# Kernel optimization log

Hardware: AMD Instinct MI355X
Metric: run time of the kernel (lower is better)

## Reference

```python
import jax, jax.numpy as jnp
import numpy as np

FP8_MAX = 448.0  # max finite value of float8_e4m3fn


def setup_inputs() -> dict:
    key = jax.random.key(0)
    k1, k2, k3 = jax.random.split(key, 3)
    T, H = 8192, 4096
    x = jax.random.normal(k1, (T, H), dtype=jnp.float32)
    w = jax.random.uniform(k2, (H, H), dtype=jnp.float32)  # stored as fp8 in the module; quantized in reference
    wscale = jax.random.uniform(k3, (1,), dtype=jnp.float32)
    return {"x": x, "w": w, "wscale": wscale}


def reference(x, w, wscale):
    # Dynamic per-token activation quantization to fp8 e4m3 (symmetric).
    x_scale = jnp.max(jnp.abs(x), axis=-1, keepdims=True) / FP8_MAX  # [T, 1]
    x_scale = jnp.maximum(x_scale, jnp.float32(1e-12))
    x_q = jnp.clip(x / x_scale, -FP8_MAX, FP8_MAX).astype(jnp.float8_e4m3fn)
    # Weight is stored in fp8 (per-tensor scale wscale); replicate the cast.
    w_q = w.astype(jnp.float8_e4m3fn)
    # Scaled fp8 matmul with fp32 accumulation, then dequant by x_scale * wscale.
    y = jnp.einsum('tk,kh->th', x_q.astype(jnp.float32), w_q.astype(jnp.float32))
    y = y * x_scale * wscale  # [T, H]
    # tensor_model_parallel_all_reduce is identity on a single device.
    return y
```

## Files before the change

kernel.cpp:

```cpp
#include <hip/hip_runtime.h>
#include <stdint.h>

#define T_DIM 8192
#define K_DIM 4096
#define N_DIM 4096
#define FP8MAX 448.0f

typedef __attribute__((ext_vector_type(4))) float floatx4;
typedef __attribute__((ext_vector_type(2))) long longx2;


__device__ static inline void load16_g2lds(const void* gptr, void* lptr) {
    __builtin_amdgcn_global_load_lds(
        (const __attribute__((address_space(1))) void*)gptr,
        (__attribute__((address_space(3))) void*)lptr,
        16, 0, 0);
}

__device__ static inline uint32_t pack4_fp8(float f0, float f1, float f2, float f3) {
    int p = 0;
    p = __builtin_amdgcn_cvt_pk_fp8_f32(f0, f1, p, false);
    p = __builtin_amdgcn_cvt_pk_fp8_f32(f2, f3, p, true);
    return (uint32_t)p;
}

__global__ __launch_bounds__(256) void xquant_kernel(
    const float* __restrict__ x, uint8_t* __restrict__ xq,
    float* __restrict__ xscale)
{
    const int t = blockIdx.x;
    const int tid = threadIdx.x;
    const int lane = tid & 63;
    const int wave = tid >> 6;
    const float4* xr4 = (const float4*)(x + (size_t)t * K_DIM);

    float4 v[4];
    float m = 0.0f;
#pragma unroll
    for (int e = 0; e < 4; ++e) {
        v[e] = xr4[tid + e * 256];
        m = fmaxf(m, fmaxf(fmaxf(fabsf(v[e].x), fabsf(v[e].y)),
                           fmaxf(fabsf(v[e].z), fabsf(v[e].w))));
    }
#pragma unroll
    for (int off = 32; off > 0; off >>= 1)
        m = fmaxf(m, __shfl_down(m, off, 64));
    __shared__ float red[4];
    if (lane == 0) red[wave] = m;
    __syncthreads();
    float mm = fmaxf(fmaxf(red[0], red[1]), fmaxf(red[2], red[3]));
    float scale = fmaxf(mm / FP8MAX, 1e-12f);
    if (tid == 0) xscale[t] = scale;
    const float inv = 1.0f / scale;

    uint32_t* xqr = (uint32_t*)(xq + (size_t)t * K_DIM);
#pragma unroll
    for (int e = 0; e < 4; ++e) {
        float q0 = fminf(fmaxf(v[e].x * inv, -FP8MAX), FP8MAX);
        float q1 = fminf(fmaxf(v[e].y * inv, -FP8MAX), FP8MAX);
        float q2 = fminf(fmaxf(v[e].z * inv, -FP8MAX), FP8MAX);
        float q3 = fminf(fmaxf(v[e].w * inv, -FP8MAX), FP8MAX);
        xqr[tid + e * 256] = pack4_fp8(q0, q1, q2, q3);
    }
}

__global__ __launch_bounds__(256) void wquant_kernel(
    const float* __restrict__ w, uint8_t* __restrict__ wqT)
{
    const int n0 = blockIdx.x * 64;
    const int k0 = blockIdx.y * 64;
    __shared__ __align__(4) uint8_t tile[64][68];

#pragma unroll
    for (int e = 0; e < 4; ++e) {
        int idx = threadIdx.x + e * 256;
        int r = idx >> 4;
        int c4 = idx & 15;
        float4 v = *(const float4*)(w + (size_t)(k0 + r) * N_DIM + n0 + c4 * 4);
        uint32_t p = pack4_fp8(v.x, v.y, v.z, v.w);
        tile[c4 * 4 + 0][r] = (uint8_t)(p);
        tile[c4 * 4 + 1][r] = (uint8_t)(p >> 8);
        tile[c4 * 4 + 2][r] = (uint8_t)(p >> 16);
        tile[c4 * 4 + 3][r] = (uint8_t)(p >> 24);
    }
    __syncthreads();
#pragma unroll
    for (int e = 0; e < 4; ++e) {
        int idx = threadIdx.x + e * 256;
        int rr = idx >> 4;
        int cc = idx & 15;
        uint32_t u = *(const uint32_t*)&tile[rr][cc * 4];
        *(uint32_t*)(wqT + (size_t)(n0 + rr) * K_DIM + k0 + cc * 4) = u;
    }
}

__global__ __launch_bounds__(256) void gemm_fp8_kernel(
    const uint8_t* __restrict__ xq, const uint8_t* __restrict__ wqT,
    const float* __restrict__ xscale, const float* __restrict__ wscale,
    float* __restrict__ out)
{
    __shared__ __align__(16) uint8_t As[128 * 64];
    __shared__ __align__(16) uint8_t Bs[128 * 64];

    const int tid = threadIdx.x;
    const int lane = tid & 63;
    const int wave = tid >> 6;
    const int m0 = blockIdx.y * 128;
    const int n0 = blockIdx.x * 128;
    const int wm = (wave >> 1) * 64;
    const int wn = (wave & 1) * 64;
    const int row = lane & 15;
    const int quad = lane >> 4;

    floatx4 acc[4][4] = {{{0.f,0.f,0.f,0.f}}};

    const int c0 = tid, c1 = tid + 256;
    const int r0 = c0 >> 2, g0 = (c0 & 3) ^ (r0 & 3);
    const int r1 = c1 >> 2, g1 = (c1 & 3) ^ (r1 & 3);
    const uint8_t* gA0 = xq  + (size_t)(m0 + r0) * K_DIM + g0 * 16;
    const uint8_t* gA1 = xq  + (size_t)(m0 + r1) * K_DIM + g1 * 16;
    const uint8_t* gB0 = wqT + (size_t)(n0 + r0) * K_DIM + g0 * 16;
    const uint8_t* gB1 = wqT + (size_t)(n0 + r1) * K_DIM + g1 * 16;
    uint8_t* lA0 = As + c0 * 16;
    uint8_t* lA1 = As + c1 * 16;
    uint8_t* lB0 = Bs + c0 * 16;
    uint8_t* lB1 = Bs + c1 * 16;

    int aoff[4], boff[4];
#pragma unroll
    for (int i = 0; i < 4; ++i) {
        const int mr = wm + i * 16 + row;
        const int nr = wn + i * 16 + row;
        aoff[i] = mr * 64 + ((quad ^ (mr & 3)) << 4);
        boff[i] = nr * 64 + ((quad ^ (nr & 3)) << 4);
    }

    for (int k0 = 0; k0 < K_DIM; k0 += 64) {
        __syncthreads();
        load16_g2lds(gA0 + k0, lA0);
        load16_g2lds(gA1 + k0, lA1);
        load16_g2lds(gB0 + k0, lB0);
        load16_g2lds(gB1 + k0, lB1);
        __syncthreads();

        longx2 a[4], b[4];
#pragma unroll
        for (int i = 0; i < 4; ++i) a[i] = *(const longx2*)(As + aoff[i]);
#pragma unroll
        for (int j = 0; j < 4; ++j) b[j] = *(const longx2*)(Bs + boff[j]);
#pragma unroll
        for (int i = 0; i < 4; ++i)
#pragma unroll
            for (int j = 0; j < 4; ++j) {
                acc[i][j] = __builtin_amdgcn_mfma_f32_16x16x32_fp8_fp8(
                    a[i].x, b[j].x, acc[i][j], 0, 0, 0);
                acc[i][j] = __builtin_amdgcn_mfma_f32_16x16x32_fp8_fp8(
                    a[i].y, b[j].y, acc[i][j], 0, 0, 0);
            }
    }

    const float wsv = wscale[0];
#pragma unroll
    for (int i = 0; i < 4; ++i) {
        const int rbase = m0 + wm + i * 16 + quad * 4;
        float s[4];
#pragma unroll
        for (int r = 0; r < 4; ++r) s[r] = xscale[rbase + r] * wsv;
#pragma unroll
        for (int j = 0; j < 4; ++j) {
            const int col = n0 + wn + j * 16 + row;
#pragma unroll
            for (int r = 0; r < 4; ++r)
                out[(size_t)(rbase + r) * N_DIM + col] = acc[i][j][r] * s[r];
        }
    }
}


extern "C" void kernel_launch(void* const* d_in, const int* in_sizes, int n_in,
                              void* d_out, int out_size, void* d_ws, size_t ws_size,
                              hipStream_t stream) {
    const float* x      = (const float*)d_in[0];
    const float* w      = (const float*)d_in[1];
    const float* wscale = (const float*)d_in[2];
    float* out = (float*)d_out;

    uint8_t* xq  = (uint8_t*)d_ws;
    uint8_t* wqT = xq + (size_t)T_DIM * K_DIM;
    float* xscale = (float*)(wqT + (size_t)N_DIM * K_DIM);

    xquant_kernel<<<T_DIM, 256, 0, stream>>>(x, xq, xscale);
    wquant_kernel<<<dim3(N_DIM / 64, K_DIM / 64), 256, 0, stream>>>(w, wqT);
    gemm_fp8_kernel<<<dim3(N_DIM / 128, T_DIM / 128), 256, 0, stream>>>(
        xq, wqT, xscale, wscale, out);
}
```

Baseline: 473.5 us.

## Use gfx950 16x16x128 scaled MFMA with 128-wide K tiles and faster weight transpose

Replaces the pair of 16x16x32 fp8 MFMAs with a single 16x16x128 scaled f8f6f4 MFMA (unit scales 0x7F), doubling the K tile to 128 and widening the LDS swizzle to 8 groups. It also rewrites the weight quantize/transpose to store packed words into LDS and transpose bytes in registers, avoiding byte-wise LDS stores. The aim is higher MFMA throughput and fewer barriers per K step, at the cost of doubled LDS use per block, which may lower occupancy.

```diff
diff --git a/kernel.cpp b/kernel.cpp
--- a/kernel.cpp
+++ b/kernel.cpp
@@ -7,7 +7,8 @@
 #define FP8MAX 448.0f
 
 typedef __attribute__((ext_vector_type(4))) float floatx4;
-typedef __attribute__((ext_vector_type(2))) long longx2;
+typedef __attribute__((ext_vector_type(4))) int   intx4;
+typedef __attribute__((ext_vector_type(8))) int   intx8;
 
 
 __device__ static inline void load16_g2lds(const void* gptr, void* lptr) {
@@ -69,7 +70,7 @@
 {
     const int n0 = blockIdx.x * 64;
     const int k0 = blockIdx.y * 64;
-    __shared__ __align__(4) uint8_t tile[64][68];
+    __shared__ uint32_t tile[64][17];
 
 #pragma unroll
     for (int e = 0; e < 4; ++e) {
@@ -77,20 +78,22 @@
         int r = idx >> 4;
         int c4 = idx & 15;
         float4 v = *(const float4*)(w + (size_t)(k0 + r) * N_DIM + n0 + c4 * 4);
-        uint32_t p = pack4_fp8(v.x, v.y, v.z, v.w);
-        tile[c4 * 4 + 0][r] = (uint8_t)(p);
-        tile[c4 * 4 + 1][r] = (uint8_t)(p >> 8);
-        tile[c4 * 4 + 2][r] = (uint8_t)(p >> 16);
-        tile[c4 * 4 + 3][r] = (uint8_t)(p >> 24);
+        tile[r][c4] = pack4_fp8(v.x, v.y, v.z, v.w);
     }
     __syncthreads();
-#pragma unroll
-    for (int e = 0; e < 4; ++e) {
-        int idx = threadIdx.x + e * 256;
-        int rr = idx >> 4;
-        int cc = idx & 15;
-        uint32_t u = *(const uint32_t*)&tile[rr][cc * 4];
-        *(uint32_t*)(wqT + (size_t)(n0 + rr) * K_DIM + k0 + cc * 4) = u;
+    const int kg = threadIdx.x & 15;
+    const int ng = threadIdx.x >> 4;
+    uint32_t in0 = tile[kg * 4 + 0][ng];
+    uint32_t in1 = tile[kg * 4 + 1][ng];
+    uint32_t in2 = tile[kg * 4 + 2][ng];
+    uint32_t in3 = tile[kg * 4 + 3][ng];
+#pragma unroll
+    for (int i = 0; i < 4; ++i) {
+        uint32_t o = ((in0 >> (8 * i)) & 0xFFu)
+                   | (((in1 >> (8 * i)) & 0xFFu) << 8)
+                   | (((in2 >> (8 * i)) & 0xFFu) << 16)
+                   | (((in3 >> (8 * i)) & 0xFFu) << 24);
+        *(uint32_t*)(wqT + (size_t)(n0 + ng * 4 + i) * K_DIM + k0 + kg * 4) = o;
     }
 }
 
@@ -99,8 +102,8 @@
     const float* __restrict__ xscale, const float* __restrict__ wscale,
     float* __restrict__ out)
 {
-    __shared__ __align__(16) uint8_t As[128 * 64];
-    __shared__ __align__(16) uint8_t Bs[128 * 64];
+    __shared__ __align__(16) uint8_t As[128 * 128];
+    __shared__ __align__(16) uint8_t Bs[128 * 128];
 
     const int tid = threadIdx.x;
     const int lane = tid & 63;
@@ -114,49 +117,62 @@
 
     floatx4 acc[4][4] = {{{0.f,0.f,0.f,0.f}}};
 
-    const int c0 = tid, c1 = tid + 256;
-    const int r0 = c0 >> 2, g0 = (c0 & 3) ^ (r0 & 3);
-    const int r1 = c1 >> 2, g1 = (c1 & 3) ^ (r1 & 3);
-    const uint8_t* gA0 = xq  + (size_t)(m0 + r0) * K_DIM + g0 * 16;
-    const uint8_t* gA1 = xq  + (size_t)(m0 + r1) * K_DIM + g1 * 16;
-    const uint8_t* gB0 = wqT + (size_t)(n0 + r0) * K_DIM + g0 * 16;
-    const uint8_t* gB1 = wqT + (size_t)(n0 + r1) * K_DIM + g1 * 16;
-    uint8_t* lA0 = As + c0 * 16;
-    uint8_t* lA1 = As + c1 * 16;
-    uint8_t* lB0 = Bs + c0 * 16;
-    uint8_t* lB1 = Bs + c1 * 16;
-
-    int aoff[4], boff[4];
+    const uint8_t* gA[4];
+    const uint8_t* gB[4];
+    uint8_t* lA[4];
+    uint8_t* lB[4];
+#pragma unroll
+    for (int p = 0; p < 4; ++p) {
+        const int c = tid + p * 256;
+        const int r = c >> 3, gg = c & 7, g = gg ^ (r & 7);
+        gA[p] = xq  + (size_t)(m0 + r) * K_DIM + g * 16;
+        gB[p] = wqT + (size_t)(n0 + r) * K_DIM + g * 16;
+        lA[p] = As + c * 16;
+        lB[p] = Bs + c * 16;
+    }
+
+    int aoff0[4], aoff1[4], boff0[4], boff1[4];
 #pragma unroll
     for (int i = 0; i < 4; ++i) {
         const int mr = wm + i * 16 + row;
         const int nr = wn + i * 16 + row;
-        aoff[i] = mr * 64 + ((quad ^ (mr & 3)) << 4);
-        boff[i] = nr * 64 + ((quad ^ (nr & 3)) << 4);
-    }
-
-    for (int k0 = 0; k0 < K_DIM; k0 += 64) {
+        aoff0[i] = mr * 128 + (((2 * quad)     ^ (mr & 7)) << 4);
+        aoff1[i] = mr * 128 + (((2 * quad + 1) ^ (mr & 7)) << 4);
+        boff0[i] = nr * 128 + (((2 * quad)     ^ (nr & 7)) << 4);
+        boff1[i] = nr * 128 + (((2 * quad + 1) ^ (nr & 7)) << 4);
+    }
+
+    for (int k0 = 0; k0 < K_DIM; k0 += 128) {
         __syncthreads();
-        load16_g2lds(gA0 + k0, lA0);
-        load16_g2lds(gA1 + k0, lA1);
-        load16_g2lds(gB0 + k0, lB0);
-        load16_g2lds(gB1 + k0, lB1);
+#pragma unroll
+        for (int p = 0; p < 4; ++p) {
+            load16_g2lds(gA[p] + k0, lA[p]);
+            load16_g2lds(gB[p] + k0, lB[p]);
+        }
         __syncthreads();
 
-        longx2 a[4], b[4];
-#pragma unroll
-        for (int i = 0; i < 4; ++i) a[i] = *(const longx2*)(As + aoff[i]);
-#pragma unroll
-        for (int j = 0; j < 4; ++j) b[j] = *(const longx2*)(Bs + boff[j]);
+        intx8 a[4], b[4];
+#pragma unroll
+        for (int i = 0; i < 4; ++i) {
+            intx4 lo = *(const intx4*)(As + aoff0[i]);
+            intx4 hi = *(const intx4*)(As + aoff1[i]);
+            a[i] = __builtin_shufflevector(lo, hi, 0, 1, 2, 3, 4, 5, 6, 7);
+        }
+#pragma unroll
+        for (int j = 0; j < 4; ++j) {
+            intx4 lo = *(const intx4*)(Bs + boff0[j]);
+            intx4 hi = *(const intx4*)(Bs + boff1[j]);
+            b[j] = __builtin_shufflevector(lo, hi, 0, 1, 2, 3, 4, 5, 6, 7);
+        }
 #pragma unroll
         for (int i = 0; i < 4; ++i)
 #pragma unroll
-            for (int j = 0; j < 4; ++j) {
-                acc[i][j] = __builtin_amdgcn_mfma_f32_16x16x32_fp8_fp8(
-                    a[i].x, b[j].x, acc[i][j], 0, 0, 0);
-                acc[i][j] = __builtin_amdgcn_mfma_f32_16x16x32_fp8_fp8(
-                    a[i].y, b[j].y, acc[i][j], 0, 0, 0);
-            }
+            for (int j = 0; j < 4; ++j)
+                acc[i][j] = __builtin_amdgcn_mfma_scale_f32_16x16x128_f8f6f4(
+                    a[i], b[j], acc[i][j],
+                    0, 0,
+                    0, 0x7F7F7F7F,
+                    0, 0x7F7F7F7F);
     }
 
     const float wsv = wscale[0];
```

Result: faster. 408.4 us (-13.7%).
